# Kernel tuning notes

Hardware: AMD Instinct MI355X
Metric: run time of the kernel (lower is better)

The kernel has to match this reference:

```python
import jax, jax.numpy as jnp
import numpy as np


def setup_inputs() -> dict:
    key = jax.random.key(0)
    k_x, k_idx, k_sgn = jax.random.split(key, 3)
    batch, original_dim, proj_dim, c = 32, 1000000, 4096, 8
    x = jax.random.normal(k_x, (batch, original_dim), dtype=jnp.float32)
    rand_indices = jax.random.randint(k_idx, (original_dim, c), 0, proj_dim, dtype=jnp.int32)
    # random signs in {-1, +1}, matching torch.randint(0,2)*2-1 cast to int8
    rand_signs = (jax.random.randint(k_sgn, (original_dim, c), 0, 2, dtype=jnp.int32) * 2 - 1)
    return {"x": x, "rand_indices": rand_indices, "rand_signs": rand_signs,
            "proj_dim": proj_dim, "c": c}


def reference(x, rand_indices, rand_signs, proj_dim, c):
    # SJLT: each input coordinate d is scattered to c random output buckets
    # with random sign; normalized by 1/sqrt(c) so the sketch preserves norms.
    scale = jnp.asarray(1.0 / np.sqrt(c), dtype=x.dtype)
    batch = x.shape[0]
    out = jnp.zeros((batch, proj_dim), dtype=x.dtype)
    # c is a small fixed constant; loop over it, vectorize over batch & features.
    for j in range(c):
        vals = x * rand_signs[:, j].astype(x.dtype)      # [B, D]
        out = out.at[:, rand_indices[:, j]].add(vals)     # scatter-add along proj dim
    return out * scale
```

## Files before the change

### kernel.cpp

```cpp
#include <hip/hip_runtime.h>
#include <hip/hip_fp16.h>


#define D_TOTAL 1000000
#define PROJ    4096
#define C_SK    8
#define NE      (D_TOTAL * C_SK)
#define SCALE   0.35355339059327373f

#define NSEG    16
#define SEG_D   62500
#define CAPA2   8448
#define CAP_B   192
#define BINCAP_A 96
#define BINCAP_B 96
#define TILE    4096
#define TILE_B  4352
#define NBLK_A  ((NE + TILE - 1) / TILE)
#define NBLK_T  ((D_TOTAL + 255) / 256)

#define SMEM_FUSED 25088

#define CURA_OFF    0
#define CURB_OFF    16384
#define LISTB_OFF   294912
#define LISTB_SZ    ((size_t)NSEG * PROJ * CAP_B * 4)
#define XT_OFF_R    (LISTB_OFF + LISTB_SZ)
#define XT_SZ       ((size_t)D_TOTAL * 32 * 2)
#define LISTA_OFF_R (XT_OFF_R + XT_SZ)
#define LISTA_SZ    ((size_t)NSEG * 64 * CAPA2 * 4)
#define PARTIAL_SZ  ((size_t)NSEG * PROJ * 32 * 4)
#define WS_ROOMY    (LISTA_OFF_R + LISTA_SZ)
#define PARTIAL_T   (LISTB_OFF + LISTB_SZ)
#define XTA_OFF_T   (PARTIAL_T + PARTIAL_SZ)
#define WS_TIGHT    (XTA_OFF_T + XT_SZ)

__global__ void init_cursors_kernel(int* __restrict__ curA, int* __restrict__ curB) {
    int i = blockIdx.x * blockDim.x + threadIdx.x;
    if (i < NSEG * 64) curA[i] = i * CAPA2;
    if (i < NSEG * PROJ) curB[i] = i * CAP_B;
}

template<int BC>
__device__ __forceinline__ void rank_and_stage(bool ok, int kb, int payload,
                                               int* __restrict__ cnt,
                                               int* __restrict__ stage,
                                               int* __restrict__ gcur,
                                               int* __restrict__ glist,
                                               int gcur_idx, int glim) {
    const unsigned long long valid = __ballot(ok);
    unsigned long long mask = valid;
    #pragma unroll
    for (int b = 0; b < 6; ++b) {
        const unsigned long long vote = __ballot((kb >> b) & 1);
        mask &= ((kb >> b) & 1) ? vote : ~vote;
    }
    if (ok) {
        const int lane = threadIdx.x & 63;
        const int rank = __popcll(mask & ((1ULL << lane) - 1ULL));
        const int leader = __ffsll((unsigned long long)mask) - 1;
        int base = 0;
        if (rank == 0) base = atomicAdd(&cnt[kb], __popcll(mask));
        base = __shfl(base, leader, 64);
        const int pos = base + rank;
        if (pos < BC) {
            stage[kb * BC + pos] = payload;
        } else {
            const int gp = atomicAdd(&gcur[gcur_idx], 1);
            if (gp < glim) glist[gp] = payload;
        }
    }
}

template<int BC>
__device__ __forceinline__ void flush_bins(int* __restrict__ cnt,
                                           int* __restrict__ basek,
                                           const int* __restrict__ stage,
                                           int* __restrict__ gcur,
                                           int* __restrict__ glist,
                                           int gidx0, int capPer) {
    const int tid = threadIdx.x;
    if (tid < 64) {
        const int m = min(cnt[tid], BC);
        cnt[tid]   = m;
        basek[tid] = atomicAdd(&gcur[gidx0 + tid], m);
    }
    __syncthreads();
    const int w = tid >> 6, lane = tid & 63;
    #pragma unroll 1
    for (int bi = 0; bi < 16; ++bi) {
        const int kb  = w * 16 + bi;
        const int m   = cnt[kb];
        const int gb  = basek[kb];
        const int lim = (gidx0 + kb + 1) * capPer;
        for (int i = lane; i < m; i += 64)
            if (gb + i < lim) glist[gb + i] = stage[kb * BC + i];
    }
}

__device__ __forceinline__ void pass_a_body(int abid, char* smem,
                                            const int* __restrict__ idx,
                                            const int* __restrict__ sgn,
                                            int* __restrict__ curA,
                                            int* __restrict__ listA) {
    int* stage = (int*)smem;
    int* cnt   = (int*)(smem + 64 * BINCAP_A * 4);
    int* basek = cnt + 64;
    const int tid = threadIdx.x;
    if (tid < 64) cnt[tid] = 0;
    __syncthreads();

    const int d_lo = abid * 512;
    const int seg  = d_lo / SEG_D;
    const bool boundary = ((d_lo + 511) / SEG_D) != seg;
    const int v0 = abid * (TILE / 4);

    #pragma unroll 1
    for (int k = 0; k < TILE / 1024; ++k) {
        const int vi = v0 + k * 256 + tid;
        const bool okv = vi < NE / 4;
        int4 i4 = {0,0,0,0}, s4 = {0,0,0,0};
        if (okv) { i4 = ((const int4*)idx)[vi]; s4 = ((const int4*)sgn)[vi]; }
        const int g0 = vi * 4;
        #pragma unroll
        for (int m = 0; m < 4; ++m) {
            const int bucket = (m == 0) ? i4.x : (m == 1) ? i4.y : (m == 2) ? i4.z : i4.w;
            const int sg     = (m == 0) ? s4.x : (m == 1) ? s4.y : (m == 2) ? s4.z : s4.w;
            const int kb = okv ? (bucket >> 6) : 0;
            const int payload = (g0 + m) | ((bucket & 63) << 24)
                              | (int)((unsigned)sg & 0x80000000u);
            if (!boundary) {
                rank_and_stage<BINCAP_A>(okv, kb, payload, cnt, stage, curA, listA,
                                         seg * 64 + kb, (seg * 64 + kb + 1) * CAPA2);
            } else if (okv) {
                const int segE = ((g0 + m) >> 3) / SEG_D;
                const int bin  = segE * 64 + kb;
                const int gp = atomicAdd(&curA[bin], 1);
                if (gp < (bin + 1) * CAPA2) listA[gp] = payload;
            }
        }
    }
    __syncthreads();
    flush_bins<BINCAP_A>(cnt, basek, stage, curA, listA, seg * 64, CAPA2);
}

__device__ __forceinline__ void transpose_body(int tbid, char* smem,
                                               const float* __restrict__ x,
                                               unsigned short* __restrict__ xT) {
    unsigned short (*tile)[260] = (unsigned short(*)[260])smem;
    const int tid = threadIdx.x;
    const int d0  = tbid * 256;
    const int row = tid >> 3;
    const int c8  = tid & 7;

    if (d0 + 256 <= D_TOTAL) {
        #pragma unroll
        for (int k = 0; k < 8; ++k) {
            const int c = (c8 + 8 * k) * 4;
            const float4 v = *(const float4*)(x + (size_t)row * D_TOTAL + d0 + c);
            unsigned short h[4];
            h[0] = __half_as_ushort(__float2half(v.x));
            h[1] = __half_as_ushort(__float2half(v.y));
            h[2] = __half_as_ushort(__float2half(v.z));
            h[3] = __half_as_ushort(__float2half(v.w));
            *(uint2*)&tile[row][c] = *(const uint2*)h;
        }
    } else {
        for (int k = 0; k < 8; ++k) {
            const int c = (c8 + 8 * k) * 4;
            for (int m = 0; m < 4; ++m) {
                const int d = d0 + c + m;
                tile[row][c + m] = __half_as_ushort(
                    __float2half((d < D_TOTAL) ? x[(size_t)row * D_TOTAL + d] : 0.f));
            }
        }
    }
    __syncthreads();

    const int part = tid & 3;
    #pragma unroll
    for (int k = 0; k < 4; ++k) {
        const int dl = k * 64 + (tid >> 2);
        if (d0 + dl < D_TOTAL) {
            unsigned short h[8];
            #pragma unroll
            for (int i = 0; i < 8; ++i)
                h[i] = tile[part * 8 + i][dl];
            *(uint4*)(xT + ((size_t)(d0 + dl)) * 32 + part * 8) = *(const uint4*)h;
        }
    }
}

__global__ __launch_bounds__(256, 6)
void pass_a_transpose_kernel(const int* __restrict__ idx, const int* __restrict__ sgn,
                             int* __restrict__ curA, int* __restrict__ listA,
                             const float* __restrict__ x, unsigned short* __restrict__ xT) {
    __shared__ char smem[SMEM_FUSED];
    const int id = blockIdx.x;
    if ((id % 3 == 0) && (id / 3 < NBLK_A)) {
        pass_a_body(id / 3, smem, idx, sgn, curA, listA);
    } else {
        const int tbid = id - id / 3 - ((id % 3) ? 1 : 0);
        if (tbid < NBLK_T) transpose_body(tbid, smem, x, xT);
    }
}

__global__ __launch_bounds__(256, 6)
void pass_a_kernel(const int* __restrict__ idx, const int* __restrict__ sgn,
                   int* __restrict__ curA, int* __restrict__ listA) {
    __shared__ char smem[SMEM_FUSED];
    pass_a_body(blockIdx.x, smem, idx, sgn, curA, listA);
}

__global__ __launch_bounds__(256, 6)
void transpose_kernel(const float* __restrict__ x, unsigned short* __restrict__ xT) {
    __shared__ char smem[16640];
    transpose_body(blockIdx.x, smem, x, xT);
}

__global__ __launch_bounds__(256, 6)
void pass_b_kernel(const int* __restrict__ curA, const int* __restrict__ listA,
                   int* __restrict__ curB, int* __restrict__ listB) {
    __shared__ int stage[64 * BINCAP_B];
    __shared__ int cnt[64];
    __shared__ int basek[64];
    const int tid  = threadIdx.x;
    const int part = blockIdx.x >> 1;
    const int tile = blockIdx.x & 1;
    if (tid < 64) cnt[tid] = 0;
    __syncthreads();

    const int pstart = part * CAPA2;
    const int pcount = min(curA[part] - pstart, CAPA2);
    const int t0 = tile * TILE_B;
    const int t1 = min(t0 + TILE_B, pcount);

    #pragma unroll 1
    for (int k = 0; k < TILE_B / 256; ++k) {
        const int i  = t0 + k * 256 + tid;
        const bool ok = i < t1;
        const int e  = ok ? listA[pstart + i] : 0;
        const int kb = ok ? ((e >> 24) & 63) : 0;
        const int payload = e & 0x807FFFFF;
        rank_and_stage<BINCAP_B>(ok, kb, payload, cnt, stage, curB, listB,
                                 part * 64 + kb, (part * 64 + kb + 1) * CAP_B);
    }
    __syncthreads();
    flush_bins<BINCAP_B>(cnt, basek, stage, curB, listB, part * 64, CAP_B);
}

__global__ __launch_bounds__(256, 8)
void gather_seg_kernel(const int* __restrict__ curB, const int* __restrict__ listB,
                       const unsigned short* __restrict__ xT,
                       float* __restrict__ partial) {
    __shared__ int lst[4][CAP_B];
    const int tid  = threadIdx.x;
    const int w    = tid >> 6;
    const int lane = tid & 63;
    const int gid  = blockIdx.x;
    const int k    = gid & 7;
    const int j    = gid >> 3;
    const int seg  = k + 8 * (j >> 10);
    const int p    = (j & 1023) * 4 + w;
    const int bin  = seg * PROJ + p;
    const int start = bin * CAP_B;
    const int n     = min(curB[bin] - start, CAP_B);

    for (int i = lane; i < n; i += 64) lst[w][i] = listB[start + i];

    const int slot = lane >> 2;
    const int bq   = lane & 3;
    float a0=0.f,a1=0.f,a2=0.f,a3=0.f,a4=0.f,a5=0.f,a6=0.f,a7=0.f;
    #pragma unroll 2
    for (int base = 0; base < n; base += 16) {
        const int  e  = base + slot;
        const bool ok = e < n;
        const int  pl = lst[w][ok ? e : 0];
        int d = (pl & 0x7FFFFF) >> 3;
        d = min(d, D_TOTAL - 1);
        const float s = ok ? ((pl < 0) ? -1.f : 1.f) : 0.f;
        const uint4 hv = *(const uint4*)(xT + (size_t)d * 32 + bq * 8);
        float2 f;
        f = __half22float2(*(const __half2*)&hv.x); a0 = fmaf(s, f.x, a0); a1 = fmaf(s, f.y, a1);
        f = __half22float2(*(const __half2*)&hv.y); a2 = fmaf(s, f.x, a2); a3 = fmaf(s, f.y, a3);
        f = __half22float2(*(const __half2*)&hv.z); a4 = fmaf(s, f.x, a4); a5 = fmaf(s, f.y, a5);
        f = __half22float2(*(const __half2*)&hv.w); a6 = fmaf(s, f.x, a6); a7 = fmaf(s, f.y, a7);
    }
    #pragma unroll
    for (int m = 4; m <= 32; m <<= 1) {
        a0 += __shfl_xor(a0, m, 64); a1 += __shfl_xor(a1, m, 64);
        a2 += __shfl_xor(a2, m, 64); a3 += __shfl_xor(a3, m, 64);
        a4 += __shfl_xor(a4, m, 64); a5 += __shfl_xor(a5, m, 64);
        a6 += __shfl_xor(a6, m, 64); a7 += __shfl_xor(a7, m, 64);
    }
    if (lane < 4) {
        float v[8] = {a0,a1,a2,a3,a4,a5,a6,a7};
        float* dst = partial + (size_t)bin * 32 + lane * 8;
        #pragma unroll
        for (int i = 0; i < 8; ++i) dst[i] = v[i];
    }
}

__global__ __launch_bounds__(256)
void reduce_kernel(const float* __restrict__ partial, float* __restrict__ out) {
    const int gtid = blockIdx.x * 256 + threadIdx.x;
    const int p = gtid & (PROJ - 1);
    const int b = gtid >> 12;
    float s = 0.f;
    #pragma unroll
    for (int sg = 0; sg < NSEG; ++sg)
        s += partial[((size_t)(sg * PROJ + p)) * 32 + b];
    out[(size_t)b * PROJ + p] = s * SCALE;
}

#define BG 8
#define NCHUNK 64
#define BLOCK 1024
__global__ __launch_bounds__(BLOCK, 4)
void sjlt_scatter_fallback(const float* __restrict__ x,
                           const int* __restrict__ idx,
                           const int* __restrict__ sgn,
                           float* __restrict__ out) {
    __shared__ float acc[BG * PROJ];
    const int tid = threadIdx.x;
    #pragma unroll
    for (int i = 0; i < (BG * PROJ) / BLOCK; ++i) acc[i * BLOCK + tid] = 0.0f;
    __syncthreads();
    const int chunk = D_TOTAL / NCHUNK;
    const int d0 = blockIdx.x * chunk;
    const int d1 = d0 + chunk;
    const int bg = blockIdx.y * BG;
    for (int d = d0 + tid; d < d1; d += BLOCK) {
        const int4 i0 = *(const int4*)(idx + (size_t)d * C_SK);
        const int4 i1 = *(const int4*)(idx + (size_t)d * C_SK + 4);
        const int4 s0 = *(const int4*)(sgn + (size_t)d * C_SK);
        const int4 s1 = *(const int4*)(sgn + (size_t)d * C_SK + 4);
        #pragma unroll
        for (int b = 0; b < BG; ++b) {
            const float xv = __builtin_nontemporal_load(x + (size_t)(bg + b) * D_TOTAL + d);
            const unsigned xb = __float_as_uint(xv);
            float* accb = acc + b * PROJ;
            atomicAdd(accb + i0.x, __uint_as_float(xb ^ ((unsigned)s0.x & 0x80000000u)));
            atomicAdd(accb + i0.y, __uint_as_float(xb ^ ((unsigned)s0.y & 0x80000000u)));
            atomicAdd(accb + i0.z, __uint_as_float(xb ^ ((unsigned)s0.z & 0x80000000u)));
            atomicAdd(accb + i0.w, __uint_as_float(xb ^ ((unsigned)s0.w & 0x80000000u)));
            atomicAdd(accb + i1.x, __uint_as_float(xb ^ ((unsigned)s1.x & 0x80000000u)));
            atomicAdd(accb + i1.y, __uint_as_float(xb ^ ((unsigned)s1.y & 0x80000000u)));
            atomicAdd(accb + i1.z, __uint_as_float(xb ^ ((unsigned)s1.z & 0x80000000u)));
            atomicAdd(accb + i1.w, __uint_as_float(xb ^ ((unsigned)s1.w & 0x80000000u)));
        }
    }
    __syncthreads();
    #pragma unroll
    for (int i = 0; i < (BG * PROJ) / BLOCK; ++i) {
        const int lin = i * BLOCK + tid;
        const int b = lin >> 12;
        const int pp = lin & (PROJ - 1);
        unsafeAtomicAdd(out + (size_t)(bg + b) * PROJ + pp, acc[lin] * SCALE);
    }
}

extern "C" void kernel_launch(void* const* d_in, const int* in_sizes, int n_in,
                              void* d_out, int out_size, void* d_ws, size_t ws_size,
                              hipStream_t stream) {
    const float* x   = (const float*)d_in[0];
    const int*   idx = (const int*)d_in[1];
    const int*   sgn = (const int*)d_in[2];
    float*       out = (float*)d_out;

    if (ws_size < WS_TIGHT) {
        (void)hipMemsetAsync(out, 0, (size_t)out_size * sizeof(float), stream);
        dim3 grid(NCHUNK, 32 / BG);
        sjlt_scatter_fallback<<<grid, BLOCK, 0, stream>>>(x, idx, sgn, out);
        return;
    }

    char* ws = (char*)d_ws;
    int* curA  = (int*)(ws + CURA_OFF);
    int* curB  = (int*)(ws + CURB_OFF);
    int* listB = (int*)(ws + LISTB_OFF);

    init_cursors_kernel<<<256, 256, 0, stream>>>(curA, curB);

    if (ws_size >= WS_ROOMY) {
        unsigned short* xT      = (unsigned short*)(ws + XT_OFF_R);
        int*            listA   = (int*)(ws + LISTA_OFF_R);
        float*          partial = (float*)(ws + LISTA_OFF_R);
        pass_a_transpose_kernel<<<NBLK_A + NBLK_T, 256, 0, stream>>>(
            idx, sgn, curA, listA, x, xT);
        pass_b_kernel<<<2048, 256, 0, stream>>>(curA, listA, curB, listB);
        gather_seg_kernel<<<NSEG * PROJ / 4, 256, 0, stream>>>(curB, listB, xT, partial);
        reduce_kernel<<<(32 * PROJ) / 256, 256, 0, stream>>>(partial, out);
    } else {
        float*          partial = (float*)(ws + PARTIAL_T);
        unsigned short* xT      = (unsigned short*)(ws + XTA_OFF_T);
        int*            listA   = (int*)(ws + XTA_OFF_T);
        pass_a_kernel<<<NBLK_A, 256, 0, stream>>>(idx, sgn, curA, listA);
        pass_b_kernel<<<2048, 256, 0, stream>>>(curA, listA, curB, listB);
        transpose_kernel<<<NBLK_T, 256, 0, stream>>>(x, xT);
        gather_seg_kernel<<<NSEG * PROJ / 4, 256, 0, stream>>>(curB, listB, xT, partial);
        reduce_kernel<<<(32 * PROJ) / 256, 256, 0, stream>>>(partial, out);
    }
}
```

Baseline: 358.0 us.

## Fuse second binning pass into gather using shared-memory bins per partition half

Removes the separate pass_b kernel and its global listB/curB buffers. Each gather block now bins one half of a first-level partition into 64 shared-memory bins and gathers from them directly, writing per-half partials that the reduce kernel sums. Bin overflow falls back to per-element global atomics into out, which is zeroed with a memset. The ballot-based wave ranking in rank_and_stage is also replaced by plain shared atomics. This cuts one kernel launch and a global round trip, at the cost of twice as many partial slices to reduce and a possibly slow atomic overflow path.

```diff
diff --git a/kernel.cpp b/kernel.cpp
--- a/kernel.cpp
+++ b/kernel.cpp
@@ -11,34 +11,27 @@
 #define NSEG    16
 #define SEG_D   62500
 #define CAPA2   8448
-#define CAP_B   192
 #define BINCAP_A 96
-#define BINCAP_B 96
+#define CAPH    96
 #define TILE    4096
-#define TILE_B  4352
 #define NBLK_A  ((NE + TILE - 1) / TILE)
 #define NBLK_T  ((D_TOTAL + 255) / 256)
+#define NSLICE  (NSEG * 2)
 
 #define SMEM_FUSED 25088
 
-#define CURA_OFF    0
-#define CURB_OFF    16384
-#define LISTB_OFF   294912
-#define LISTB_SZ    ((size_t)NSEG * PROJ * CAP_B * 4)
-#define XT_OFF_R    (LISTB_OFF + LISTB_SZ)
-#define XT_SZ       ((size_t)D_TOTAL * 32 * 2)
-#define LISTA_OFF_R (XT_OFF_R + XT_SZ)
-#define LISTA_SZ    ((size_t)NSEG * 64 * CAPA2 * 4)
-#define PARTIAL_SZ  ((size_t)NSEG * PROJ * 32 * 4)
-#define WS_ROOMY    (LISTA_OFF_R + LISTA_SZ)
-#define PARTIAL_T   (LISTB_OFF + LISTB_SZ)
-#define XTA_OFF_T   (PARTIAL_T + PARTIAL_SZ)
-#define WS_TIGHT    (XTA_OFF_T + XT_SZ)
-
-__global__ void init_cursors_kernel(int* __restrict__ curA, int* __restrict__ curB) {
+#define CURA_OFF   0
+#define XT_OFF     16384
+#define XT_SZ      ((size_t)D_TOTAL * 32 * 2)
+#define LISTA_OFF  (XT_OFF + XT_SZ)
+#define LISTA_SZ   ((size_t)NSEG * 64 * CAPA2 * 4)
+#define PART_OFF   (LISTA_OFF + LISTA_SZ)
+#define PART_SZ    ((size_t)NSLICE * PROJ * 32 * 4)
+#define WS_NEED    (PART_OFF + PART_SZ)
+
+__global__ void init_cursors_kernel(int* __restrict__ curA) {
     int i = blockIdx.x * blockDim.x + threadIdx.x;
     if (i < NSEG * 64) curA[i] = i * CAPA2;
-    if (i < NSEG * PROJ) curB[i] = i * CAP_B;
 }
 
 template<int BC>
@@ -48,21 +41,8 @@
                                                int* __restrict__ gcur,
                                                int* __restrict__ glist,
                                                int gcur_idx, int glim) {
-    const unsigned long long valid = __ballot(ok);
-    unsigned long long mask = valid;
-    #pragma unroll
-    for (int b = 0; b < 6; ++b) {
-        const unsigned long long vote = __ballot((kb >> b) & 1);
-        mask &= ((kb >> b) & 1) ? vote : ~vote;
-    }
     if (ok) {
-        const int lane = threadIdx.x & 63;
-        const int rank = __popcll(mask & ((1ULL << lane) - 1ULL));
-        const int leader = __ffsll((unsigned long long)mask) - 1;
-        int base = 0;
-        if (rank == 0) base = atomicAdd(&cnt[kb], __popcll(mask));
-        base = __shfl(base, leader, 64);
-        const int pos = base + rank;
+        const int pos = atomicAdd(&cnt[kb], 1);
         if (pos < BC) {
             stage[kb * BC + pos] = payload;
         } else {
@@ -206,98 +186,85 @@
 }
 
 __global__ __launch_bounds__(256, 6)
-void pass_a_kernel(const int* __restrict__ idx, const int* __restrict__ sgn,
-                   int* __restrict__ curA, int* __restrict__ listA) {
-    __shared__ char smem[SMEM_FUSED];
-    pass_a_body(blockIdx.x, smem, idx, sgn, curA, listA);
-}
-
-__global__ __launch_bounds__(256, 6)
-void transpose_kernel(const float* __restrict__ x, unsigned short* __restrict__ xT) {
-    __shared__ char smem[16640];
-    transpose_body(blockIdx.x, smem, x, xT);
-}
-
-__global__ __launch_bounds__(256, 6)
-void pass_b_kernel(const int* __restrict__ curA, const int* __restrict__ listA,
-                   int* __restrict__ curB, int* __restrict__ listB) {
-    __shared__ int stage[64 * BINCAP_B];
+void gather_part_kernel(const int* __restrict__ curA, const int* __restrict__ listA,
+                        const unsigned short* __restrict__ xT,
+                        float* __restrict__ partial, float* __restrict__ out) {
+    __shared__ int stage[64 * CAPH];
     __shared__ int cnt[64];
-    __shared__ int basek[64];
-    const int tid  = threadIdx.x;
-    const int part = blockIdx.x >> 1;
-    const int tile = blockIdx.x & 1;
+    const int tid = threadIdx.x;
+    const int gid = blockIdx.x;
+    const int seg  = (gid & 7) + 8 * (gid >> 10);
+    const int rest = (gid >> 3) & 127;
+    const int kbA  = rest >> 1;
+    const int half = rest & 1;
+    const int part = seg * 64 + kbA;
+
     if (tid < 64) cnt[tid] = 0;
     __syncthreads();
 
     const int pstart = part * CAPA2;
     const int pcount = min(curA[part] - pstart, CAPA2);
-    const int t0 = tile * TILE_B;
-    const int t1 = min(t0 + TILE_B, pcount);
-
-    #pragma unroll 1
-    for (int k = 0; k < TILE_B / 256; ++k) {
-        const int i  = t0 + k * 256 + tid;
-        const bool ok = i < t1;
-        const int e  = ok ? listA[pstart + i] : 0;
-        const int kb = ok ? ((e >> 24) & 63) : 0;
-        const int payload = e & 0x807FFFFF;
-        rank_and_stage<BINCAP_B>(ok, kb, payload, cnt, stage, curB, listB,
-                                 part * 64 + kb, (part * 64 + kb + 1) * CAP_B);
-    }
-    __syncthreads();
-    flush_bins<BINCAP_B>(cnt, basek, stage, curB, listB, part * 64, CAP_B);
-}
-
-__global__ __launch_bounds__(256, 8)
-void gather_seg_kernel(const int* __restrict__ curB, const int* __restrict__ listB,
-                       const unsigned short* __restrict__ xT,
-                       float* __restrict__ partial) {
-    __shared__ int lst[4][CAP_B];
-    const int tid  = threadIdx.x;
+    const int hn = (pcount + 1) >> 1;
+    const int t0 = half * hn;
+    const int t1 = min(t0 + hn, pcount);
+
+    for (int i = t0 + tid; i < t1; i += 256) {
+        const int e  = listA[pstart + i];
+        const int kb = (e >> 24) & 63;
+        const int pos = atomicAdd(&cnt[kb], 1);
+        if (pos < CAPH) {
+            stage[kb * CAPH + pos] = e;
+        } else {
+            int d = (e & 0x7FFFFF) >> 3;
+            d = min(d, D_TOTAL - 1);
+            const float s = (e < 0) ? -SCALE : SCALE;
+            const int p = kbA * 64 + kb;
+            for (int b = 0; b < 32; ++b) {
+                const float v = __half2float(*(const __half*)(xT + (size_t)d * 32 + b));
+                unsafeAtomicAdd(out + (size_t)b * PROJ + p, s * v);
+            }
+        }
+    }
+    __syncthreads();
+
     const int w    = tid >> 6;
     const int lane = tid & 63;
-    const int gid  = blockIdx.x;
-    const int k    = gid & 7;
-    const int j    = gid >> 3;
-    const int seg  = k + 8 * (j >> 10);
-    const int p    = (j & 1023) * 4 + w;
-    const int bin  = seg * PROJ + p;
-    const int start = bin * CAP_B;
-    const int n     = min(curB[bin] - start, CAP_B);
-
-    for (int i = lane; i < n; i += 64) lst[w][i] = listB[start + i];
-
     const int slot = lane >> 2;
     const int bq   = lane & 3;
-    float a0=0.f,a1=0.f,a2=0.f,a3=0.f,a4=0.f,a5=0.f,a6=0.f,a7=0.f;
-    #pragma unroll 2
-    for (int base = 0; base < n; base += 16) {
-        const int  e  = base + slot;
-        const bool ok = e < n;
-        const int  pl = lst[w][ok ? e : 0];
-        int d = (pl & 0x7FFFFF) >> 3;
-        d = min(d, D_TOTAL - 1);
-        const float s = ok ? ((pl < 0) ? -1.f : 1.f) : 0.f;
-        const uint4 hv = *(const uint4*)(xT + (size_t)d * 32 + bq * 8);
-        float2 f;
-        f = __half22float2(*(const __half2*)&hv.x); a0 = fmaf(s, f.x, a0); a1 = fmaf(s, f.y, a1);
-        f = __half22float2(*(const __half2*)&hv.y); a2 = fmaf(s, f.x, a2); a3 = fmaf(s, f.y, a3);
-        f = __half22float2(*(const __half2*)&hv.z); a4 = fmaf(s, f.x, a4); a5 = fmaf(s, f.y, a5);
-        f = __half22float2(*(const __half2*)&hv.w); a6 = fmaf(s, f.x, a6); a7 = fmaf(s, f.y, a7);
-    }
-    #pragma unroll
-    for (int m = 4; m <= 32; m <<= 1) {
-        a0 += __shfl_xor(a0, m, 64); a1 += __shfl_xor(a1, m, 64);
-        a2 += __shfl_xor(a2, m, 64); a3 += __shfl_xor(a3, m, 64);
-        a4 += __shfl_xor(a4, m, 64); a5 += __shfl_xor(a5, m, 64);
-        a6 += __shfl_xor(a6, m, 64); a7 += __shfl_xor(a7, m, 64);
-    }
-    if (lane < 4) {
-        float v[8] = {a0,a1,a2,a3,a4,a5,a6,a7};
-        float* dst = partial + (size_t)bin * 32 + lane * 8;
+    #pragma unroll 1
+    for (int bi = 0; bi < 16; ++bi) {
+        const int kb = w * 16 + bi;
+        const int n  = min(cnt[kb], CAPH);
+        float a0=0.f,a1=0.f,a2=0.f,a3=0.f,a4=0.f,a5=0.f,a6=0.f,a7=0.f;
+        #pragma unroll 2
+        for (int base = 0; base < n; base += 16) {
+            const int  e  = base + slot;
+            const bool ok = e < n;
+            const int  pl = stage[kb * CAPH + (ok ? e : 0)];
+            int d = (pl & 0x7FFFFF) >> 3;
+            d = min(d, D_TOTAL - 1);
+            const float s = ok ? ((pl < 0) ? -1.f : 1.f) : 0.f;
+            const uint4 hv = *(const uint4*)(xT + (size_t)d * 32 + bq * 8);
+            float2 f;
+            f = __half22float2(*(const __half2*)&hv.x); a0 = fmaf(s, f.x, a0); a1 = fmaf(s, f.y, a1);
+            f = __half22float2(*(const __half2*)&hv.y); a2 = fmaf(s, f.x, a2); a3 = fmaf(s, f.y, a3);
+            f = __half22float2(*(const __half2*)&hv.z); a4 = fmaf(s, f.x, a4); a5 = fmaf(s, f.y, a5);
+            f = __half22float2(*(const __half2*)&hv.w); a6 = fmaf(s, f.x, a6); a7 = fmaf(s, f.y, a7);
+        }
         #pragma unroll
-        for (int i = 0; i < 8; ++i) dst[i] = v[i];
+        for (int m = 4; m <= 32; m <<= 1) {
+            a0 += __shfl_xor(a0, m, 64); a1 += __shfl_xor(a1, m, 64);
+            a2 += __shfl_xor(a2, m, 64); a3 += __shfl_xor(a3, m, 64);
+            a4 += __shfl_xor(a4, m, 64); a5 += __shfl_xor(a5, m, 64);
+            a6 += __shfl_xor(a6, m, 64); a7 += __shfl_xor(a7, m, 64);
+        }
+        if (lane < 4) {
+            float v[8] = {a0,a1,a2,a3,a4,a5,a6,a7};
+            const size_t slice = (size_t)(seg * 2 + half);
+            float* dst = partial + (slice * PROJ + (size_t)(kbA * 64 + kb)) * 32 + lane * 8;
+            #pragma unroll
+            for (int i = 0; i < 8; ++i) dst[i] = v[i];
+        }
     }
 }
 
@@ -308,9 +275,10 @@
     const int b = gtid >> 12;
     float s = 0.f;
     #pragma unroll
-    for (int sg = 0; sg < NSEG; ++sg)
+    for (int sg = 0; sg < NSLICE; ++sg)
         s += partial[((size_t)(sg * PROJ + p)) * 32 + b];
-    out[(size_t)b * PROJ + p] = s * SCALE;
+    const size_t o = (size_t)b * PROJ + p;
+    out[o] = out[o] + s * SCALE;
 }
 
 #define BG 8
@@ -368,7 +336,7 @@
     const int*   sgn = (const int*)d_in[2];
     float*       out = (float*)d_out;
 
-    if (ws_size < WS_TIGHT) {
+    if (ws_size < WS_NEED) {
         (void)hipMemsetAsync(out, 0, (size_t)out_size * sizeof(float), stream);
         dim3 grid(NCHUNK, 32 / BG);
         sjlt_scatter_fallback<<<grid, BLOCK, 0, stream>>>(x, idx, sgn, out);
@@ -376,29 +344,15 @@
     }
 
     char* ws = (char*)d_ws;
-    int* curA  = (int*)(ws + CURA_OFF);
-    int* curB  = (int*)(ws + CURB_OFF);
-    int* listB = (int*)(ws + LISTB_OFF);
-
-    init_cursors_kernel<<<256, 256, 0, stream>>>(curA, curB);
-
-    if (ws_size >= WS_ROOMY) {
-        unsigned short* xT      = (unsigned short*)(ws + XT_OFF_R);
-        int*            listA   = (int*)(ws + LISTA_OFF_R);
-        float*          partial = (float*)(ws + LISTA_OFF_R);
-        pass_a_transpose_kernel<<<NBLK_A + NBLK_T, 256, 0, stream>>>(
-            idx, sgn, curA, listA, x, xT);
-        pass_b_kernel<<<2048, 256, 0, stream>>>(curA, listA, curB, listB);
-        gather_seg_kernel<<<NSEG * PROJ / 4, 256, 0, stream>>>(curB, listB, xT, partial);
-        reduce_kernel<<<(32 * PROJ) / 256, 256, 0, stream>>>(partial, out);
-    } else {
-        float*          partial = (float*)(ws + PARTIAL_T);
-        unsigned short* xT      = (unsigned short*)(ws + XTA_OFF_T);
-        int*            listA   = (int*)(ws + XTA_OFF_T);
-        pass_a_kernel<<<NBLK_A, 256, 0, stream>>>(idx, sgn, curA, listA);
-        pass_b_kernel<<<2048, 256, 0, stream>>>(curA, listA, curB, listB);
-        transpose_kernel<<<NBLK_T, 256, 0, stream>>>(x, xT);
-        gather_seg_kernel<<<NSEG * PROJ / 4, 256, 0, stream>>>(curB, listB, xT, partial);
-        reduce_kernel<<<(32 * PROJ) / 256, 256, 0, stream>>>(partial, out);
-    }
-}
+    int*            curA    = (int*)(ws + CURA_OFF);
+    unsigned short* xT      = (unsigned short*)(ws + XT_OFF);
+    int*            listA   = (int*)(ws + LISTA_OFF);
+    float*          partial = (float*)(ws + PART_OFF);
+
+    (void)hipMemsetAsync(out, 0, (size_t)out_size * sizeof(float), stream);
+    init_cursors_kernel<<<4, 256, 0, stream>>>(curA);
+    pass_a_transpose_kernel<<<NBLK_A + NBLK_T, 256, 0, stream>>>(
+        idx, sgn, curA, listA, x, xT);
+    gather_part_kernel<<<2048, 256, 0, stream>>>(curA, listA, xT, partial, out);
+    reduce_kernel<<<(32 * PROJ) / 256, 256, 0, stream>>>(partial, out);
+}
```

After: 370.4 us. 1.03x slower.
